# Optimization experiments

Measured on AMD Instinct MI355X. Metric: run time of the kernel, lower is better.

Reference implementation:

```python
import jax, jax.numpy as jnp
import numpy as np

B, K, N, M = 32, 128, 128, 256  # batch, num_classes(==n_dim), n_dim, samples-per-matrix
EPSILON = 0.1
LAMBDA_SOFTMAX = 0.1
LEARNING_RATE = 0.01
BN_EPS = 1e-5


def setup_inputs() -> dict:
    key = jax.random.key(0)
    k1, k2, k3 = jax.random.split(key, 3)
    x = jax.random.normal(k1, (B, N, M), dtype=jnp.float32)
    A = jax.random.normal(k2, (K, N, N), dtype=jnp.float32) * 0.1
    EC_proto = jnp.einsum('kij,klj->kil', A, A)  # per-class PSD prototype covariances (K,N,N)
    EC_count = jax.random.uniform(k3, (K,), dtype=jnp.float32, minval=1.0, maxval=100.0)
    return {"x": x, "EC_proto": EC_proto, "EC_count": EC_count}


def reference(x, EC_proto, EC_count):
    n = x.shape[1]
    dtype = x.dtype
    # BatchNorm1d(num_classes, affine=False, track_running_stats=False): batch stats over (N, L)
    mean = x.mean(axis=(0, 2), keepdims=True)
    var = x.var(axis=(0, 2), keepdims=True)  # biased variance, as torch uses for normalization
    x = (x - mean) / jnp.sqrt(var + BN_EPS)

    eye = jnp.eye(n, dtype=dtype)
    total = EC_count.sum()
    has_counts = total > 1e-6

    # E branch: global expansion operator
    e_alpha = jnp.where(has_counts, n / (EPSILON * EPSILON * total), jnp.zeros((), dtype))
    e = e_alpha * jnp.linalg.inv(e_alpha * EC_proto.sum(0) + eye)  # (N,N)
    e_x_z = jnp.einsum('ij,bjm->bim', e, x)  # (B,N,M)

    # C branch: per-class compression operators
    bool_depth = (EC_count != 0).astype(dtype)  # (K,)
    count_fix = EC_count + (1.0 - bool_depth)
    c_alpha = (n / (count_fix * EPSILON * EPSILON) * bool_depth)[:, None, None]  # (K,1,1)
    c = c_alpha * jnp.linalg.inv(c_alpha * EC_proto + eye[None])  # (K,N,N)
    c_x_z = jnp.einsum('kij,bjm->bkim', c, x)  # (B,K,N,M)

    # Frobenius norm per (b,k), rescaled to sum to 10 over classes
    norm = jnp.sqrt((c_x_z * c_x_z).sum(axis=(2, 3)))  # (B,K)
    norm = 10.0 * norm / norm.sum(axis=1, keepdims=True)

    pi = jax.nn.softmax(-LAMBDA_SOFTMAX * norm, axis=1) * bool_depth  # (B,K)
    gama = jnp.where(has_counts, EC_count / total, jnp.zeros_like(EC_count))  # (K,)

    z_d = e_x_z - jnp.einsum('k,bkim,bk->bim', gama, c_x_z, pi)  # (B,N,M)
    return x + LEARNING_RATE * z_d
```

## Files before the change

### kernel.cpp

```cpp
#include <hip/hip_runtime.h>
#include <math.h>

#define Bb 32
#define Kk 128
#define Nn 128
#define Mm 256
#define EPS2 0.01f
#define LAMBDA_S 0.1f
#define LR 0.01f
#define BN_EPS_C 1e-5f

#define SWZ(c) (((c) & 14) | (((c) & 1) << 4) | (((c) >> 4) & 1))

__device__ __forceinline__ float readlane_f(float v, int lane) {
  return __int_as_float(__builtin_amdgcn_readlane(__float_as_int(v), lane));
}

__global__ void kA_bn_psum(const float* __restrict__ x, const float* __restrict__ P,
                           float* __restrict__ xn, float* __restrict__ Psum) {
  int t = threadIdx.x;
  if (blockIdx.x < 128) {
    int n = blockIdx.x;
    float v[32];
    float s = 0.f, s2 = 0.f;
    #pragma unroll
    for (int b = 0; b < Bb; ++b) {
      v[b] = x[(size_t)b * (Nn * Mm) + n * Mm + t];
      s += v[b];
      s2 += v[b] * v[b];
    }
    #pragma unroll
    for (int o = 32; o > 0; o >>= 1) {
      s += __shfl_down(s, o, 64);
      s2 += __shfl_down(s2, o, 64);
    }
    __shared__ float rs[4], rs2[4];
    if ((t & 63) == 0) { rs[t >> 6] = s; rs2[t >> 6] = s2; }
    __syncthreads();
    float S = rs[0] + rs[1] + rs[2] + rs[3];
    float S2 = rs2[0] + rs2[1] + rs2[2] + rs2[3];
    float mean = S * (1.0f / (Bb * Mm));
    float var = S2 * (1.0f / (Bb * Mm)) - mean * mean;
    float rstd = 1.0f / sqrtf(var + BN_EPS_C);
    #pragma unroll
    for (int b = 0; b < Bb; ++b)
      xn[(size_t)b * (Nn * Mm) + n * Mm + t] = (v[b] - mean) * rstd;
  } else {
    int e = (blockIdx.x - 128) * 256 + t;
    float s = 0.f;
    #pragma unroll 8
    for (int k = 0; k < Kk; ++k) s += P[(size_t)k * 16384 + e];
    Psum[e] = s;
  }
}

__global__ __launch_bounds__(512, 1) void k3S(
    const float* __restrict__ P, const float* __restrict__ Psum,
    const float* __restrict__ cnt, float* __restrict__ C,
    const float* __restrict__ xn, float* __restrict__ S) {
  __shared__ __align__(16) float LB[8448];
  int bx = blockIdx.x;
  int t = threadIdx.x;

  if (bx < 65) {
    int h = t >> 8;
    int tt = t & 255;
    float* Mt = LB + h * 4224;
    float* Rb = Mt + 2112;
    float* redc = Mt + 4160;
    int mat = bx * 2 + h;
    int tx = tt & 15, ty = tt >> 4;

    float cv = cnt[tt & 127];
    float sr = cv;
    #pragma unroll
    for (int o = 32; o > 0; o >>= 1) sr += __shfl_down(sr, o, 64);
    if ((tt & 63) == 0) redc[tt >> 6] = sr;
    __syncthreads();
    float total = redc[0] + redc[1];
    bool has = total > 1e-6f;
    float av;
    if (mat < 128) {
      float c = cnt[mat];
      float bk = (c != 0.0f) ? 1.0f : 0.0f;
      float cfix = c + (1.0f - bk);
      av = (float)Nn / (cfix * EPS2) * bk;
    } else if (mat == 128) {
      av = has ? ((float)Nn / (EPS2 * total)) : 0.0f;
    } else {
      av = 0.0f;
    }
    const float* src = (mat < 128) ? (P + (size_t)mat * 16384) : Psum;

    float a[8][8];
    #pragma unroll
    for (int i = 0; i < 8; ++i) {
      int row = ty * 8 + i;
      float4 p0 = *(const float4*)&src[row * 128 + tx * 8];
      float4 p1 = *(const float4*)&src[row * 128 + tx * 8 + 4];
      a[i][0] = av * p0.x; a[i][1] = av * p0.y; a[i][2] = av * p0.z; a[i][3] = av * p0.w;
      a[i][4] = av * p1.x; a[i][5] = av * p1.y; a[i][6] = av * p1.z; a[i][7] = av * p1.w;
      if (tx == ty) a[i][i] += 1.0f;
    }

    for (int kb = 0; kb < 8; ++kb) {
      int k0 = kb * 16;
      if ((ty >> 1) == kb) {
        int d = ty & 1;
        #pragma unroll
        for (int i = 0; i < 8; ++i) {
          *(float4*)&Rb[(d * 8 + i) * 128 + SWZ(2 * tx) * 4] =
              make_float4(a[i][0], a[i][1], a[i][2], a[i][3]);
          *(float4*)&Rb[(d * 8 + i) * 128 + SWZ(2 * tx + 1) * 4] =
              make_float4(a[i][4], a[i][5], a[i][6], a[i][7]);
        }
      }
      if ((tx >> 1) == kb) {
        int dh = tx & 1;
        #pragma unroll
        for (int i = 0; i < 8; ++i)
          #pragma unroll
          for (int j = 0; j < 8; ++j)
            Mt[(dh * 8 + j) * 132 + ty * 8 + i] = a[i][j];
      }
      __syncthreads();

      if (tt < 64) {
        int l = tt;
        float m[2][16];
        #pragma unroll
        for (int d = 0; d < 2; ++d)
          #pragma unroll
          for (int j = 0; j < 16; ++j)
            m[d][j] = Mt[j * 132 + 2 * l + d];
        #pragma unroll
        for (int q = 0; q < 16; ++q) {
          int lq = (k0 + q) >> 1;
          float pr[16];
          #pragma unroll
          for (int j = 0; j < 16; ++j) pr[j] = readlane_f(m[q & 1][j], lq);
          float piv = pr[q];
          float r0 = __builtin_amdgcn_rcpf(piv);
          float pinv = r0 * (2.0f - piv * r0);
          #pragma unroll
          for (int d = 0; d < 2; ++d) {
            float f = m[d][q];
            bool isp = (2 * l + d == k0 + q);
            float g = isp ? (1.0f - pinv) : f * pinv;
            #pragma unroll
            for (int j = 0; j < 16; ++j) m[d][j] = fmaf(-g, pr[j], m[d][j]);
            m[d][q] = isp ? pinv : -g;
          }
        }
        #pragma unroll
        for (int d = 0; d < 2; ++d)
          #pragma unroll
          for (int j = 0; j < 16; ++j)
            Mt[j * 132 + 2 * l + d] = m[d][j];
      }
      __syncthreads();

      if ((ty >> 1) == kb) {
        #pragma unroll
        for (int i = 0; i < 8; ++i)
          #pragma unroll
          for (int j = 0; j < 8; ++j) a[i][j] = 0.0f;
      }
      #pragma unroll
      for (int q = 0; q < 16; ++q) {
        float4 m0 = *(const float4*)&Mt[q * 132 + ty * 8];
        float4 m1 = *(const float4*)&Mt[q * 132 + ty * 8 + 4];
        float4 r0 = *(const float4*)&Rb[q * 128 + SWZ(2 * tx) * 4];
        float4 r1 = *(const float4*)&Rb[q * 128 + SWZ(2 * tx + 1) * 4];
        float mq[8] = {m0.x, m0.y, m0.z, m0.w, m1.x, m1.y, m1.z, m1.w};
        float rq[8] = {r0.x, r0.y, r0.z, r0.w, r1.x, r1.y, r1.z, r1.w};
        #pragma unroll
        for (int i = 0; i < 8; ++i)
          #pragma unroll
          for (int j = 0; j < 8; ++j)
            a[i][j] = fmaf(mq[i], rq[j], a[i][j]);
      }
      if ((tx >> 1) == kb) {
        int dh = tx & 1;
        #pragma unroll
        for (int j = 0; j < 8; ++j) {
          float4 v0 = *(const float4*)&Mt[(dh * 8 + j) * 132 + ty * 8];
          float4 v1 = *(const float4*)&Mt[(dh * 8 + j) * 132 + ty * 8 + 4];
          a[0][j] = v0.x; a[1][j] = v0.y; a[2][j] = v0.z; a[3][j] = v0.w;
          a[4][j] = v1.x; a[5][j] = v1.y; a[6][j] = v1.z; a[7][j] = v1.w;
        }
      }
      __syncthreads();
    }

    if (mat < 129) {
      float* dst = C + (size_t)mat * 16384;
      #pragma unroll
      for (int i = 0; i < 8; ++i) {
        int row = ty * 8 + i;
        float4 v0 = make_float4(av * a[i][0], av * a[i][1], av * a[i][2], av * a[i][3]);
        float4 v1 = make_float4(av * a[i][4], av * a[i][5], av * a[i][6], av * a[i][7]);
        *(float4*)&dst[row * 128 + tx * 8] = v0;
        *(float4*)&dst[row * 128 + tx * 8 + 4] = v1;
      }
    }
  } else {
    int bxx = bx - 65;
    int b = bxx >> 1;
    int jbase = (bxx & 1) * 64;
    float* X = LB;
    int tx = t & 15, ty = (t >> 4) & 15;
    float acc[8][4] = {};
    for (int mc = 0; mc < Mm; mc += 64) {
      __syncthreads();
      #pragma unroll
      for (int c = 0; c < 16; ++c) {
        int e = c * 512 + t;
        int i = e >> 6, mm = e & 63;
        X[i * 65 + mm] = xn[(size_t)b * (Nn * Mm) + i * Mm + mc + mm];
      }
      __syncthreads();
      if (t < 256) {
        for (int mm = 0; mm < 64; ++mm) {
          float ai[8], bj[4];
          #pragma unroll
          for (int q = 0; q < 8; ++q) ai[q] = X[(ty * 8 + q) * 65 + mm];
          #pragma unroll
          for (int q = 0; q < 4; ++q) bj[q] = X[(jbase + tx * 4 + q) * 65 + mm];
          #pragma unroll
          for (int qi = 0; qi < 8; ++qi)
            #pragma unroll
            for (int qj = 0; qj < 4; ++qj)
              acc[qi][qj] = fmaf(ai[qi], bj[qj], acc[qi][qj]);
        }
      }
    }
    if (t < 256) {
      float* dst = S + (size_t)b * 16384;
      #pragma unroll
      for (int qi = 0; qi < 8; ++qi) {
        float4 v = make_float4(acc[qi][0], acc[qi][1], acc[qi][2], acc[qi][3]);
        *(float4*)&dst[(ty * 8 + qi) * 128 + jbase + tx * 4] = v;
      }
    }
  }
}

__global__ __launch_bounds__(256, 1) void kGN(const float* __restrict__ C,
                                              const float* __restrict__ S,
                                              float* __restrict__ norm2h) {
  __shared__ __align__(16) float LB[128 * 128];
  __shared__ float redb[4][32];
  int k = blockIdx.x >> 1, h = blockIdx.x & 1;
  int t = threadIdx.x;
  const float* src = C + (size_t)k * 16384;
  for (int c = 0; c < 64; ++c) LB[c * 256 + t] = src[c * 256 + t];
  __syncthreads();
  int tx = t & 15, ty = t >> 4;
  int i0 = ty * 8, j0 = h * 64 + tx * 4;
  float acc[8][4] = {};
  for (int l = 0; l < 128; ++l) {
    float ai[8], bj[4];
    *(float4*)&ai[0] = *(const float4*)&LB[l * 128 + i0];
    *(float4*)&ai[4] = *(const float4*)&LB[l * 128 + i0 + 4];
    *(float4*)&bj[0] = *(const float4*)&LB[l * 128 + j0];
    #pragma unroll
    for (int qi = 0; qi < 8; ++qi)
      #pragma unroll
      for (int qj = 0; qj < 4; ++qj)
        acc[qi][qj] = fmaf(ai[qi], bj[qj], acc[qi][qj]);
  }
  __syncthreads();
  #pragma unroll
  for (int qi = 0; qi < 8; ++qi)
    *(float4*)&LB[(i0 + qi) * 64 + tx * 4] =
        make_float4(acc[qi][0], acc[qi][1], acc[qi][2], acc[qi][3]);
  __syncthreads();
  float nacc[32];
  #pragma unroll
  for (int b = 0; b < 32; ++b) nacc[b] = 0.0f;
  #pragma unroll
  for (int q = 0; q < 8; ++q) {
    int el = (q * 256 + t) * 4;
    float4 g = *(const float4*)&LB[el];
    int i = el >> 6, jl = el & 63;
    const float* sb = S + i * 128 + h * 64 + jl;
    #pragma unroll
    for (int b = 0; b < 32; ++b) {
      float4 sv = *(const float4*)&sb[(size_t)b * 16384];
      nacc[b] = fmaf(g.x, sv.x, nacc[b]);
      nacc[b] = fmaf(g.y, sv.y, nacc[b]);
      nacc[b] = fmaf(g.z, sv.z, nacc[b]);
      nacc[b] = fmaf(g.w, sv.w, nacc[b]);
    }
  }
  #pragma unroll
  for (int b = 0; b < 32; ++b) {
    float v = nacc[b];
    #pragma unroll
    for (int o = 32; o > 0; o >>= 1) v += __shfl_down(v, o, 64);
    nacc[b] = v;
  }
  if ((t & 63) == 0) {
    int w = t >> 6;
    #pragma unroll
    for (int b = 0; b < 32; ++b) redb[w][b] = nacc[b];
  }
  __syncthreads();
  if (t < 32)
    norm2h[(size_t)k * 64 + h * 32 + t] =
        redb[0][t] + redb[1][t] + redb[2][t] + redb[3][t];
}

__global__ void k7n(const float* __restrict__ norm2h, const float* __restrict__ cnt,
                    float* __restrict__ wT) {
  int b = blockIdx.x;
  int k = threadIdx.x;
  float n2 = norm2h[(size_t)k * 64 + b] + norm2h[(size_t)k * 64 + 32 + b];
  float norm = sqrtf(fmaxf(n2, 0.0f));
  float cv = cnt[k];
  __shared__ float r1[2], r2[2], r3[2];
  float tt = cv, r = norm;
  #pragma unroll
  for (int o = 32; o > 0; o >>= 1) {
    tt += __shfl_down(tt, o, 64);
    r += __shfl_down(r, o, 64);
  }
  if ((k & 63) == 0) { r1[k >> 6] = tt; r2[k >> 6] = r; }
  __syncthreads();
  float total = r1[0] + r1[1];
  float sumn = r2[0] + r2[1];
  float nr = 10.0f * norm / fmaxf(sumn, 1e-30f);
  float ex = expf(-LAMBDA_S * nr);
  float e2 = ex;
  #pragma unroll
  for (int o = 32; o > 0; o >>= 1) e2 += __shfl_down(e2, o, 64);
  if ((k & 63) == 0) r3[k >> 6] = e2;
  __syncthreads();
  float sume = r3[0] + r3[1];
  float bk = (cv != 0.0f) ? 1.0f : 0.0f;
  float pi = (ex / sume) * bk;
  float gama = (total > 1e-6f) ? (cv / total) : 0.0f;
  wT[k * 32 + b] = gama * pi;
}

__global__ __launch_bounds__(256, 1) void k8_k(const float* __restrict__ C,
                                               const float* __restrict__ E,
                                               const float* __restrict__ wT,
                                               float* __restrict__ F) {
  int e = blockIdx.x * 256 + threadIdx.x;
  int b0 = blockIdx.y * 8;
  float acc[8];
  float ev = E[e];
  #pragma unroll
  for (int b = 0; b < 8; ++b) acc[b] = ev;
  for (int k = 0; k < 128; ++k) {
    float cv = C[(size_t)k * 16384 + e];
    const float* wk = wT + k * 32 + b0;
    #pragma unroll
    for (int b = 0; b < 8; ++b) acc[b] = fmaf(-wk[b], cv, acc[b]);
  }
  #pragma unroll
  for (int b = 0; b < 8; ++b) F[(size_t)(b0 + b) * 16384 + e] = acc[b];
}

__global__ __launch_bounds__(256, 1) void k9_k(const float* __restrict__ F,
                                               const float* __restrict__ xn,
                                               float* __restrict__ out) {
  int bx = blockIdx.x;
  int b = bx >> 3, y = bx & 7;
  int mq = y >> 1, ih = y & 1;
  __shared__ __align__(16) float Ft[64 * 68];
  __shared__ __align__(16) float Xt[64 * 68];
  int t = threadIdx.x;
  int tx = t & 15, ty = t >> 4;
  float acc[4][4] = {};
  for (int jc = 0; jc < 128; jc += 64) {
    __syncthreads();
    #pragma unroll
    for (int q = 0; q < 4; ++q) {
      int e = q * 256 + t;
      int i = e >> 4, j4 = e & 15;
      *(float4*)&Ft[i * 68 + j4 * 4] =
          *(const float4*)&F[(size_t)b * 16384 + (ih * 64 + i) * 128 + jc + j4 * 4];
    }
    #pragma unroll
    for (int q = 0; q < 4; ++q) {
      int e = q * 256 + t;
      int jj = e >> 4, m4 = e & 15;
      *(float4*)&Xt[jj * 68 + m4 * 4] =
          *(const float4*)&xn[(size_t)b * (Nn * Mm) + (jc + jj) * Mm + mq * 64 + m4 * 4];
    }
    __syncthreads();
    for (int j4 = 0; j4 < 16; ++j4) {
      float4 fi[4], xm[4];
      #pragma unroll
      for (int r = 0; r < 4; ++r)
        fi[r] = *(const float4*)&Ft[(ty * 4 + r) * 68 + j4 * 4];
      #pragma unroll
      for (int r = 0; r < 4; ++r)
        xm[r] = *(const float4*)&Xt[(j4 * 4 + r) * 68 + tx * 4];
      #pragma unroll
      for (int qi = 0; qi < 4; ++qi) {
        #pragma unroll
        for (int qm = 0; qm < 4; ++qm) {
          float xv = ((const float*)&xm[0])[qm];
          acc[qi][qm] = fmaf(fi[qi].x, xv, acc[qi][qm]);
          xv = ((const float*)&xm[1])[qm];
          acc[qi][qm] = fmaf(fi[qi].y, xv, acc[qi][qm]);
          xv = ((const float*)&xm[2])[qm];
          acc[qi][qm] = fmaf(fi[qi].z, xv, acc[qi][qm]);
          xv = ((const float*)&xm[3])[qm];
          acc[qi][qm] = fmaf(fi[qi].w, xv, acc[qi][qm]);
        }
      }
    }
  }
  int i0 = ih * 64 + ty * 4, m0 = mq * 64 + tx * 4;
  #pragma unroll
  for (int qi = 0; qi < 4; ++qi) {
    float4 xv = *(const float4*)&xn[(size_t)b * (Nn * Mm) + (i0 + qi) * Mm + m0];
    float4 o;
    o.x = fmaf(LR, acc[qi][0], xv.x);
    o.y = fmaf(LR, acc[qi][1], xv.y);
    o.z = fmaf(LR, acc[qi][2], xv.z);
    o.w = fmaf(LR, acc[qi][3], xv.w);
    *(float4*)&out[(size_t)b * (Nn * Mm) + (i0 + qi) * Mm + m0] = o;
  }
}

extern "C" void kernel_launch(void* const* d_in, const int* in_sizes, int n_in,
                              void* d_out, int out_size, void* d_ws, size_t ws_size,
                              hipStream_t stream) {
  const float* x = (const float*)d_in[0];
  const float* P = (const float*)d_in[1];
  const float* cnt = (const float*)d_in[2];
  float* out = (float*)d_out;

  float* ws = (float*)d_ws;
  float* xn = ws;
  float* C = xn + 1048576;
  float* S = C + 2113536;
  float* norm2h = S + 524288;
  float* wT = norm2h + 8192;
  float* F = wT + 4096;
  float* Psum = F + 524288;
  size_t need_bytes = (size_t)((Psum + 16384) - ws) * sizeof(float);
  if (ws_size < need_bytes) return;

  hipLaunchKernelGGL(kA_bn_psum, dim3(192), dim3(256), 0, stream, x, P, xn, Psum);
  hipLaunchKernelGGL(k3S, dim3(129), dim3(512), 0, stream, P, Psum, cnt, C, xn, S);
  hipLaunchKernelGGL(kGN, dim3(256), dim3(256), 0, stream, C, S, norm2h);
  hipLaunchKernelGGL(k7n, dim3(32), dim3(128), 0, stream, norm2h, cnt, wT);
  hipLaunchKernelGGL(k8_k, dim3(64, 4), dim3(256), 0, stream, C,
                     C + (size_t)128 * 16384, wT, F);
  hipLaunchKernelGGL(k9_k, dim3(256), dim3(256), 0, stream, F, xn, out);
}
```

Measured before the change: 193.5 us.

## Co-schedule Gram matrix computation inside idle threads of inversion blocks

Before, each inversion block inverted two matrices with 256 threads apiece, and 64 separate blocks computed the per-batch Gram matrices S. Now each block inverts one matrix with its lower 256 threads. The upper 256 threads, which used to sit idle, compute a 128x32 slice of S across the inversion's synchronisation phases, loading one chunk of xn per step. This aims to hide the Gram work behind the latency-bound Gauss-Jordan inversion and spread the inversions across more blocks. The price is a grid of 129 blocks with one matrix each, more register pressure, and a fixed coupling between the two workloads.

```diff
diff --git a/kernel.cpp b/kernel.cpp
--- a/kernel.cpp
+++ b/kernel.cpp
@@ -59,40 +59,44 @@
     const float* __restrict__ cnt, float* __restrict__ C,
     const float* __restrict__ xn, float* __restrict__ S) {
   __shared__ __align__(16) float LB[8448];
+  float* Mt = LB;
+  float* Rb = LB + 2112;
+  float* redc = LB + 4160;
+  float* X = LB + 4224;
   int bx = blockIdx.x;
   int t = threadIdx.x;
-
-  if (bx < 65) {
-    int h = t >> 8;
-    int tt = t & 255;
-    float* Mt = LB + h * 4224;
-    float* Rb = Mt + 2112;
-    float* redc = Mt + 4160;
-    int mat = bx * 2 + h;
-    int tx = tt & 15, ty = tt >> 4;
-
-    float cv = cnt[tt & 127];
+  int mat = bx;
+
+  int tx = t & 15, ty = (t >> 4) & 15;
+  float a[8][8];
+  float av = 0.f;
+  int u = t - 256;
+  int stx = u & 7, sty = u >> 3;
+  int sb = (bx < 128) ? (bx >> 2) : 0;
+  int cb = (bx & 3) * 32;
+  float acc[4][4] = {};
+
+  if (t < 256) {
+    float cv = cnt[t & 127];
     float sr = cv;
     #pragma unroll
     for (int o = 32; o > 0; o >>= 1) sr += __shfl_down(sr, o, 64);
-    if ((tt & 63) == 0) redc[tt >> 6] = sr;
-    __syncthreads();
+    if ((t & 63) == 0) redc[t >> 6] = sr;
+  }
+  __syncthreads();
+
+  if (t < 256) {
     float total = redc[0] + redc[1];
     bool has = total > 1e-6f;
-    float av;
     if (mat < 128) {
       float c = cnt[mat];
       float bk = (c != 0.0f) ? 1.0f : 0.0f;
       float cfix = c + (1.0f - bk);
       av = (float)Nn / (cfix * EPS2) * bk;
-    } else if (mat == 128) {
+    } else {
       av = has ? ((float)Nn / (EPS2 * total)) : 0.0f;
-    } else {
-      av = 0.0f;
     }
     const float* src = (mat < 128) ? (P + (size_t)mat * 16384) : Psum;
-
-    float a[8][8];
     #pragma unroll
     for (int i = 0; i < 8; ++i) {
       int row = ty * 8 + i;
@@ -102,9 +106,11 @@
       a[i][4] = av * p1.x; a[i][5] = av * p1.y; a[i][6] = av * p1.z; a[i][7] = av * p1.w;
       if (tx == ty) a[i][i] += 1.0f;
     }
-
-    for (int kb = 0; kb < 8; ++kb) {
-      int k0 = kb * 16;
+  }
+
+  for (int kb = 0; kb < 8; ++kb) {
+    int k0 = kb * 16;
+    if (t < 256) {
       if ((ty >> 1) == kb) {
         int d = ty & 1;
         #pragma unroll
@@ -123,43 +129,70 @@
           for (int j = 0; j < 8; ++j)
             Mt[(dh * 8 + j) * 132 + ty * 8 + i] = a[i][j];
       }
-      __syncthreads();
-
-      if (tt < 64) {
-        int l = tt;
-        float m[2][16];
-        #pragma unroll
-        for (int d = 0; d < 2; ++d)
-          #pragma unroll
-          for (int j = 0; j < 16; ++j)
-            m[d][j] = Mt[j * 132 + 2 * l + d];
-        #pragma unroll
-        for (int q = 0; q < 16; ++q) {
-          int lq = (k0 + q) >> 1;
-          float pr[16];
-          #pragma unroll
-          for (int j = 0; j < 16; ++j) pr[j] = readlane_f(m[q & 1][j], lq);
-          float piv = pr[q];
-          float r0 = __builtin_amdgcn_rcpf(piv);
-          float pinv = r0 * (2.0f - piv * r0);
-          #pragma unroll
-          for (int d = 0; d < 2; ++d) {
-            float f = m[d][q];
-            bool isp = (2 * l + d == k0 + q);
-            float g = isp ? (1.0f - pinv) : f * pinv;
-            #pragma unroll
-            for (int j = 0; j < 16; ++j) m[d][j] = fmaf(-g, pr[j], m[d][j]);
-            m[d][q] = isp ? pinv : -g;
-          }
+    } else {
+      int mc = kb * 32;
+      #pragma unroll
+      for (int q = 0; q < 4; ++q) {
+        int idx = q * 256 + u;
+        int row = idx >> 3, s4 = idx & 7;
+        float4 g = *(const float4*)&xn[(size_t)sb * (Nn * Mm) + row * Mm + mc + s4 * 4];
+        X[(s4 * 4 + 0) * 132 + row] = g.x;
+        X[(s4 * 4 + 1) * 132 + row] = g.y;
+        X[(s4 * 4 + 2) * 132 + row] = g.z;
+        X[(s4 * 4 + 3) * 132 + row] = g.w;
+      }
+    }
+    __syncthreads();
+
+    if (t < 64) {
+      int l = t;
+      float m[2][16];
+      #pragma unroll
+      for (int d = 0; d < 2; ++d)
+        #pragma unroll
+        for (int j = 0; j < 16; ++j)
+          m[d][j] = Mt[j * 132 + 2 * l + d];
+      #pragma unroll
+      for (int q = 0; q < 16; ++q) {
+        int lq = (k0 + q) >> 1;
+        float pr[16];
+        #pragma unroll
+        for (int j = 0; j < 16; ++j) pr[j] = readlane_f(m[q & 1][j], lq);
+        float piv = pr[q];
+        float r0 = __builtin_amdgcn_rcpf(piv);
+        float pinv = r0 * (2.0f - piv * r0);
+        #pragma unroll
+        for (int d = 0; d < 2; ++d) {
+          float f = m[d][q];
+          bool isp = (2 * l + d == k0 + q);
+          float g = isp ? (1.0f - pinv) : f * pinv;
+          #pragma unroll
+          for (int j = 0; j < 16; ++j) m[d][j] = fmaf(-g, pr[j], m[d][j]);
+          m[d][q] = isp ? pinv : -g;
         }
-        #pragma unroll
-        for (int d = 0; d < 2; ++d)
-          #pragma unroll
-          for (int j = 0; j < 16; ++j)
-            Mt[j * 132 + 2 * l + d] = m[d][j];
-      }
-      __syncthreads();
-
+      }
+      #pragma unroll
+      for (int d = 0; d < 2; ++d)
+        #pragma unroll
+        for (int j = 0; j < 16; ++j)
+          Mt[j * 132 + 2 * l + d] = m[d][j];
+    } else if (t >= 256) {
+      #pragma unroll
+      for (int mm = 0; mm < 16; ++mm) {
+        float4 ai = *(const float4*)&X[mm * 132 + sty * 4];
+        float4 bj = *(const float4*)&X[mm * 132 + cb + stx * 4];
+        float aiv[4] = {ai.x, ai.y, ai.z, ai.w};
+        float bjv[4] = {bj.x, bj.y, bj.z, bj.w};
+        #pragma unroll
+        for (int qi = 0; qi < 4; ++qi)
+          #pragma unroll
+          for (int qj = 0; qj < 4; ++qj)
+            acc[qi][qj] = fmaf(aiv[qi], bjv[qj], acc[qi][qj]);
+      }
+    }
+    __syncthreads();
+
+    if (t < 256) {
       if ((ty >> 1) == kb) {
         #pragma unroll
         for (int i = 0; i < 8; ++i)
@@ -190,58 +223,39 @@
           a[4][j] = v1.x; a[5][j] = v1.y; a[6][j] = v1.z; a[7][j] = v1.w;
         }
       }
-      __syncthreads();
-    }
-
-    if (mat < 129) {
-      float* dst = C + (size_t)mat * 16384;
-      #pragma unroll
-      for (int i = 0; i < 8; ++i) {
-        int row = ty * 8 + i;
-        float4 v0 = make_float4(av * a[i][0], av * a[i][1], av * a[i][2], av * a[i][3]);
-        float4 v1 = make_float4(av * a[i][4], av * a[i][5], av * a[i][6], av * a[i][7]);
-        *(float4*)&dst[row * 128 + tx * 8] = v0;
-        *(float4*)&dst[row * 128 + tx * 8 + 4] = v1;
-      }
-    }
-  } else {
-    int bxx = bx - 65;
-    int b = bxx >> 1;
-    int jbase = (bxx & 1) * 64;
-    float* X = LB;
-    int tx = t & 15, ty = (t >> 4) & 15;
-    float acc[8][4] = {};
-    for (int mc = 0; mc < Mm; mc += 64) {
-      __syncthreads();
-      #pragma unroll
-      for (int c = 0; c < 16; ++c) {
-        int e = c * 512 + t;
-        int i = e >> 6, mm = e & 63;
-        X[i * 65 + mm] = xn[(size_t)b * (Nn * Mm) + i * Mm + mc + mm];
-      }
-      __syncthreads();
-      if (t < 256) {
-        for (int mm = 0; mm < 64; ++mm) {
-          float ai[8], bj[4];
-          #pragma unroll
-          for (int q = 0; q < 8; ++q) ai[q] = X[(ty * 8 + q) * 65 + mm];
-          #pragma unroll
-          for (int q = 0; q < 4; ++q) bj[q] = X[(jbase + tx * 4 + q) * 65 + mm];
-          #pragma unroll
-          for (int qi = 0; qi < 8; ++qi)
-            #pragma unroll
-            for (int qj = 0; qj < 4; ++qj)
-              acc[qi][qj] = fmaf(ai[qi], bj[qj], acc[qi][qj]);
-        }
-      }
-    }
-    if (t < 256) {
-      float* dst = S + (size_t)b * 16384;
-      #pragma unroll
-      for (int qi = 0; qi < 8; ++qi) {
-        float4 v = make_float4(acc[qi][0], acc[qi][1], acc[qi][2], acc[qi][3]);
-        *(float4*)&dst[(ty * 8 + qi) * 128 + jbase + tx * 4] = v;
-      }
+    } else {
+      #pragma unroll
+      for (int mm = 16; mm < 32; ++mm) {
+        float4 ai = *(const float4*)&X[mm * 132 + sty * 4];
+        float4 bj = *(const float4*)&X[mm * 132 + cb + stx * 4];
+        float aiv[4] = {ai.x, ai.y, ai.z, ai.w};
+        float bjv[4] = {bj.x, bj.y, bj.z, bj.w};
+        #pragma unroll
+        for (int qi = 0; qi < 4; ++qi)
+          #pragma unroll
+          for (int qj = 0; qj < 4; ++qj)
+            acc[qi][qj] = fmaf(aiv[qi], bjv[qj], acc[qi][qj]);
+      }
+    }
+    __syncthreads();
+  }
+
+  if (t < 256) {
+    float* dst = C + (size_t)mat * 16384;
+    #pragma unroll
+    for (int i = 0; i < 8; ++i) {
+      int row = ty * 8 + i;
+      float4 v0 = make_float4(av * a[i][0], av * a[i][1], av * a[i][2], av * a[i][3]);
+      float4 v1 = make_float4(av * a[i][4], av * a[i][5], av * a[i][6], av * a[i][7]);
+      *(float4*)&dst[row * 128 + tx * 8] = v0;
+      *(float4*)&dst[row * 128 + tx * 8 + 4] = v1;
+    }
+  } else if (bx < 128) {
+    float* dst = S + (size_t)sb * 16384;
+    #pragma unroll
+    for (int qi = 0; qi < 4; ++qi) {
+      float4 v = make_float4(acc[qi][0], acc[qi][1], acc[qi][2], acc[qi][3]);
+      *(float4*)&dst[(sty * 4 + qi) * 128 + cb + stx * 4] = v;
     }
   }
 }
```

Result: faster. 169.7 us (-12.3%).
